# Kernel optimization log

Measured on AMD Instinct MI355X. Metric: run time of the kernel, lower is better.

## Reference

```python
import jax, jax.numpy as jnp
import numpy as np

B, S_RAW, S_SUM, D_IN, H, NH = 32, 1024, 128, 300, 256, 4
DH = (2 * H) // NH  # per-head dim = 128


def _lstm_dir(x, Wih, Whh, b, reverse):
    """Single-direction LSTM (PyTorch gate order i,f,g,o). x: [B,S,D] -> [B,S,H]."""
    xg = jnp.einsum('bsd,gd->bsg', x, Wih) + b          # precompute input gates [B,S,4H]
    xg = jnp.swapaxes(xg, 0, 1)                          # [S,B,4H]
    Hh = Whh.shape[1]
    bsz = x.shape[0]

    def step(carry, g):
        h, c = carry
        gates = g + h @ Whh.T
        i, f, gg, o = jnp.split(gates, 4, axis=-1)
        c = jax.nn.sigmoid(f) * c + jax.nn.sigmoid(i) * jnp.tanh(gg)
        h = jax.nn.sigmoid(o) * jnp.tanh(c)
        return (h, c), h

    init = (jnp.zeros((bsz, Hh), x.dtype), jnp.zeros((bsz, Hh), x.dtype))
    _, hs = jax.lax.scan(step, init, xg, reverse=reverse)  # hs aligned with input time order
    return jnp.swapaxes(hs, 0, 1)


def _bilstm(x, pf, pb):
    return jnp.concatenate([_lstm_dir(x, *pf, False), _lstm_dir(x, *pb, True)], axis=-1)


def setup_inputs() -> dict:
    key = jax.random.key(0)
    ks = jax.random.split(key, 24)
    s_lstm = 1.0 / np.sqrt(H)
    s_proj = 1.0 / np.sqrt(2 * H)
    d = {}
    d['in_raw'] = jax.random.normal(ks[0], (B, S_RAW, D_IN), jnp.float32)
    d['in_sum'] = jax.random.normal(ks[1], (B, S_SUM, D_IN), jnp.float32)
    d['len_raw'] = jax.random.randint(ks[2], (B,), 0, S_RAW)
    d['len_sum'] = jax.random.randint(ks[3], (B,), 0, S_SUM)
    i = 4
    for name in ['raw_f', 'raw_b', 'sum_f', 'sum_b']:
        d[name + '_Wih'] = jax.random.uniform(ks[i], (4 * H, D_IN), jnp.float32, -s_lstm, s_lstm); i += 1
        d[name + '_Whh'] = jax.random.uniform(ks[i], (4 * H, H), jnp.float32, -s_lstm, s_lstm); i += 1
        d[name + '_b'] = jax.random.uniform(ks[i], (4 * H,), jnp.float32, -s_lstm, s_lstm); i += 1
    d['Wq'] = jax.random.uniform(ks[i], (NH, 2 * H, DH), jnp.float32, -s_proj, s_proj); i += 1
    d['Wk'] = jax.random.uniform(ks[i], (NH, 2 * H, DH), jnp.float32, -s_proj, s_proj); i += 1
    d['Wv'] = jax.random.uniform(ks[i], (NH, 2 * H, DH), jnp.float32, -s_proj, s_proj)
    return d


def reference(in_raw, in_sum, len_raw, len_sum,
              raw_f_Wih, raw_f_Whh, raw_f_b, raw_b_Wih, raw_b_Whh, raw_b_b,
              sum_f_Wih, sum_f_Whh, sum_f_b, sum_b_Wih, sum_b_Whh, sum_b_b,
              Wq, Wk, Wv):
    # BiLSTM encoders (dropout is identity in eval mode)
    out_raw = _bilstm(in_raw, (raw_f_Wih, raw_f_Whh, raw_f_b), (raw_b_Wih, raw_b_Whh, raw_b_b))  # [B,Sr,2H]
    out_sum = _bilstm(in_sum, (sum_f_Wih, sum_f_Whh, sum_f_b), (sum_b_Wih, sum_b_Whh, sum_b_b))  # [B,Ss,2H]

    # mean_pooling over the first len_sum[i] timesteps (lengths clamped to >=1)
    lens = jnp.maximum(len_sum, 1)
    mask = (jnp.arange(S_SUM)[None, :] < lens[:, None]).astype(out_sum.dtype)  # [B,Ss]
    sum_vec = jnp.einsum('bsd,bs->bd', out_sum, mask) / lens.astype(out_sum.dtype)[:, None]  # [B,2H]

    # per-head cross-attention against the single pooled summary vector (rank-1 attention)
    q = jnp.einsum('bsd,hde->hbse', out_raw, Wq)   # [NH,B,Sr,DH]
    k = jnp.einsum('bd,hde->hbe', sum_vec, Wk)     # [NH,B,DH]
    v = jnp.einsum('bd,hde->hbe', sum_vec, Wv)     # [NH,B,DH]
    scores = jnp.einsum('hbse,hbe->hbs', q, k)     # [NH,B,Sr] (use_divide_dk=False)
    attn = jax.nn.softmax(scores, axis=-1)
    rst = attn[..., None] * v[:, :, None, :] + q   # outer product + residual, [NH,B,Sr,DH]

    # concat heads along last dim -> [B,Sr,2H]
    rst = jnp.transpose(rst, (1, 2, 0, 3)).reshape(B, S_RAW, NH * DH)
    return rst
```

## Files before the change

kernel.cpp:

```cpp
#include <hip/hip_runtime.h>

typedef _Float16 f16;
typedef _Float16 half2t __attribute__((ext_vector_type(2)));
typedef _Float16 half8 __attribute__((ext_vector_type(8)));
typedef float f32x4 __attribute__((ext_vector_type(4)));

#define KP 320
#define DIN 300
#define SRAW 1024
#define SSUM 128

static constexpr size_t OFF_XG_RAW  = 0;
static constexpr size_t OFF_XG_SUM  = OFF_XG_RAW + (size_t)2*32*1024*1024*2;
static constexpr size_t OFF_OUT_RAW = OFF_XG_SUM + (size_t)2*32*128*1024*2;
static constexpr size_t OFF_OUT_SUM = OFF_OUT_RAW + (size_t)32*1024*512*2;
static constexpr size_t OFF_A_RAW   = OFF_OUT_SUM + (size_t)32*128*512*2;
static constexpr size_t OFF_A_SUM   = OFF_A_RAW + (size_t)32768*KP*2;
static constexpr size_t OFF_BIH_RAW = OFF_A_SUM + (size_t)4096*KP*2;
static constexpr size_t OFF_BIH_SUM = OFF_BIH_RAW + (size_t)2048*KP*2;
static constexpr size_t OFF_WHH     = OFF_BIH_SUM + (size_t)2048*KP*2;
static constexpr size_t OFF_WQ      = OFF_WHH + (size_t)4*32*1024*8*2;
static constexpr size_t OFF_KB      = OFF_WQ + (size_t)512*512*2;
static constexpr size_t OFF_VB      = OFF_KB + (size_t)4*32*128*4;
static constexpr size_t OFF_ATTN    = OFF_VB + (size_t)4*32*128*4;
static constexpr size_t WS_NEED     = OFF_ATTN + (size_t)4*32*1024*4;

__global__ void pack_kernel(
    const float* __restrict__ in_raw, const float* __restrict__ in_sum,
    const float* __restrict__ wih_rf, const float* __restrict__ wih_rb,
    const float* __restrict__ wih_sf, const float* __restrict__ wih_sb,
    const float* __restrict__ whh_rf, const float* __restrict__ whh_rb,
    const float* __restrict__ whh_sf, const float* __restrict__ whh_sb,
    const float* __restrict__ wq,
    f16* __restrict__ a_raw, f16* __restrict__ a_sum,
    f16* __restrict__ bih_raw, f16* __restrict__ bih_sum,
    f16* __restrict__ whh16, f16* __restrict__ wq16)
{
  constexpr size_t N1 = (size_t)32768*KP;
  constexpr size_t N2 = (size_t)4096*KP;
  constexpr size_t N3 = (size_t)2048*KP;
  constexpr size_t N5 = (size_t)4*32*1024*8;
  constexpr size_t N6 = (size_t)512*512;
  const size_t TOT = N1+N2+N3+N3+N5+N6;
  const size_t stride = (size_t)gridDim.x*blockDim.x;
  for (size_t i = (size_t)blockIdx.x*blockDim.x + threadIdx.x; i < TOT; i += stride) {
    size_t j = i;
    if (j < N1) {
      size_t m = j/KP, k = j - m*KP;
      a_raw[j] = (f16)(k < DIN ? in_raw[m*DIN + k] : 0.f);
      continue;
    }
    j -= N1;
    if (j < N2) {
      size_t m = j/KP, k = j - m*KP;
      a_sum[j] = (f16)(k < DIN ? in_sum[m*DIN + k] : 0.f);
      continue;
    }
    j -= N2;
    if (j < N3) {
      size_t n = j/KP, k = j - n*KP;
      float v = 0.f;
      if (k < DIN) v = (n < 1024) ? wih_rf[n*DIN + k] : wih_rb[(n-1024)*DIN + k];
      bih_raw[j] = (f16)v;
      continue;
    }
    j -= N3;
    if (j < N3) {
      size_t n = j/KP, k = j - n*KP;
      float v = 0.f;
      if (k < DIN) v = (n < 1024) ? wih_sf[n*DIN + k] : wih_sb[(n-1024)*DIN + k];
      bih_sum[j] = (f16)v;
      continue;
    }
    j -= N3;
    if (j < N5) {
      int ed = (int)(j >> 18);
      int c  = (int)((j >> 13) & 31);
      int t  = (int)((j >> 3) & 1023);
      int ii = (int)(j & 7);
      int jrow = c >> 2, q = c & 3;
      int rg = t >> 3, ks = t & 7;
      int row = rg*8 + jrow;
      int col = ks*32 + q*8 + ii;
      const float* src = (ed==0)?whh_rf:(ed==1)?whh_rb:(ed==2)?whh_sf:whh_sb;
      whh16[j] = (f16)src[(size_t)row*256 + col];
      continue;
    }
    j -= N5;
    {
      int n = (int)(j >> 9), k = (int)(j & 511);
      int h = n >> 7, dh = n & 127;
      wq16[j] = (f16)wq[((size_t)h*512 + k)*128 + dh];
    }
  }
}

template<int EPI>
__global__ __launch_bounds__(256) void gemm_kernel(
    const f16* __restrict__ A, const f16* __restrict__ Bm,
    float* __restrict__ Cf, f16* __restrict__ Cx,
    const float* __restrict__ bias0, const float* __restrict__ bias1,
    int K, int ldcN, size_t dirStride)
{
  __shared__ __align__(16) f16 As[128*40];
  __shared__ __align__(16) f16 Bs[128*40];
  const int tid = threadIdx.x;
  const int m0 = blockIdx.x*128, n0 = blockIdx.y*128;
  const int w = tid >> 6, lane = tid & 63;
  const int wm = w >> 1, wn = w & 1;
  const int lr = lane & 15, lk = lane >> 4;
  f32x4 acc[4][4] = {};
  const int nsteps = K >> 5;
  for (int kt = 0; kt < nsteps; ++kt) {
    __syncthreads();
    #pragma unroll
    for (int it = 0; it < 2; ++it) {
      int c = tid + it*256;
      int r = c >> 2, kc = c & 3;
      *(uint4*)&As[r*40 + kc*8] = *(const uint4*)&A[(size_t)(m0+r)*K + kt*32 + kc*8];
      *(uint4*)&Bs[r*40 + kc*8] = *(const uint4*)&Bm[(size_t)(n0+r)*K + kt*32 + kc*8];
    }
    __syncthreads();
    half8 af[4], bf[4];
    #pragma unroll
    for (int mt = 0; mt < 4; ++mt) af[mt] = *(const half8*)&As[(wm*64 + mt*16 + lr)*40 + lk*8];
    #pragma unroll
    for (int nt = 0; nt < 4; ++nt) bf[nt] = *(const half8*)&Bs[(wn*64 + nt*16 + lr)*40 + lk*8];
    #pragma unroll
    for (int mt = 0; mt < 4; ++mt)
      #pragma unroll
      for (int nt = 0; nt < 4; ++nt)
        acc[mt][nt] = __builtin_amdgcn_mfma_f32_16x16x32_f16(af[mt], bf[nt], acc[mt][nt], 0, 0, 0);
  }
  const int rb = lk*4;
  #pragma unroll
  for (int mt = 0; mt < 4; ++mt) {
    #pragma unroll
    for (int nt = 0; nt < 4; ++nt) {
      int n = n0 + wn*64 + nt*16 + lr;
      int mloc = m0 + wm*64 + mt*16 + rb;
      if (EPI == 0) {
        #pragma unroll
        for (int r = 0; r < 4; ++r)
          Cf[(size_t)(mloc+r)*ldcN + n] = acc[mt][nt][r];
      } else {
        int dir = n >> 10, cc = n & 1023;
        float bs = (dir ? bias1 : bias0)[cc];
        f16* dst = Cx + (size_t)dir*dirStride;
        #pragma unroll
        for (int r = 0; r < 4; ++r)
          dst[(size_t)(mloc+r)*1024 + cc] = (f16)(acc[mt][nt][r] + bs);
      }
    }
  }
}


__device__ __forceinline__ float dot8(float acc, uint4 wv, uint4 hv) {
#if __has_builtin(__builtin_amdgcn_fdot2)
  union { uint4 u; half2t h[4]; } W, Hh;
  W.u = wv; Hh.u = hv;
  #pragma unroll
  for (int i = 0; i < 4; ++i) acc = __builtin_amdgcn_fdot2(W.h[i], Hh.h[i], acc, false);
#else
  union { uint4 u; f16 h[8]; } W, Hh;
  W.u = wv; Hh.u = hv;
  #pragma unroll
  for (int i = 0; i < 8; ++i) acc += (float)W.h[i]*(float)Hh.h[i];
#endif
  return acc;
}

__device__ __forceinline__ float sigmoid_f(float x) {
  float e = __expf(-x);
  return __builtin_amdgcn_rcpf(1.f + e);
}
__device__ __forceinline__ float tanh_f(float x) {
  float e = __expf(2.f * x);
  return 1.f - 2.f * __builtin_amdgcn_rcpf(e + 1.f);
}

__device__ __forceinline__ void pin4(uint4& v) {
  asm volatile("" : "+v"(v.x), "+v"(v.y), "+v"(v.z), "+v"(v.w));
}

template<int CTRL>
__device__ __forceinline__ float dpp_add(float v) {
  int m = __builtin_amdgcn_update_dpp(0, __builtin_bit_cast(int, v), CTRL, 0xf, 0xf, true);
  return v + __builtin_bit_cast(float, m);
}
__device__ __forceinline__ float reduce8(float v) {
  v = dpp_add<0xB1>(v);
  v = dpp_add<0x4E>(v);
  v = dpp_add<0x141>(v);
  return v;
}

__global__ void __launch_bounds__(1024)
lstm_kernel(
    const f16* __restrict__ whh16,
    const f16* __restrict__ xg_raw, const f16* __restrict__ xg_sum,
    f16* __restrict__ out_raw, f16* __restrict__ out_sum)
{
  const int wg = blockIdx.x;
  const int e = wg >> 6, r2 = wg & 63, d = r2 >> 5, b = r2 & 31;
  const int S = e ? SSUM : SRAW;
  const int t = threadIdx.x;
  const int ks = t & 7;
  const uint4* wb = (const uint4*)(whh16 + (size_t)(e*2+d)*(32*1024*8));
  const f16* xg = (e ? xg_sum : xg_raw) + ((size_t)(d*32 + b))*(size_t)S*1024;
  f16* outp = (e ? out_sum : out_raw) + (size_t)b*S*512 + d*256;

  __shared__ __align__(16) uint4 wl[2*4*1024];
  __shared__ float pre[1024];
  __shared__ __align__(16) f16 hrep[4*264];

  #pragma unroll
  for (int c = 0; c < 8; ++c) wl[c*1024 + t] = wb[(12 + c)*1024 + t];
  uint4 wr[12];
  #pragma unroll
  for (int c = 0; c < 12; ++c) wr[c] = wb[c*1024 + t];
  #pragma unroll
  for (int c = 0; c < 12; ++c) pin4(wr[c]);

  if (t < 256) {
    #pragma unroll
    for (int cpy = 0; cpy < 4; ++cpy) hrep[cpy*264 + t] = (f16)0.f;
  }
  float cst = 0.f;
  const int hbyte = (ks >> 1)*528 + ks*64;
  const bool isG = ((t >> 8) == 2);
  __syncthreads();

  for (int st = 0; st < S; ++st) {
    const int s = d ? (S - 1 - st) : st;

    float xv = (float)xg[(size_t)s*1024 + t];

    uint4 g5[4];
    #pragma unroll
    for (int q = 0; q < 4; ++q) g5[q] = wb[(20 + q)*1024 + t];

    uint4 hv[4];
    #pragma unroll
    for (int q = 0; q < 4; ++q)
      hv[q] = *(const uint4*)((const char*)hrep + hbyte + q*16);

    float pa = 0.f;

    #pragma unroll
    for (int j = 0; j < 3; ++j) {
      float rs = 0.f;
      #pragma unroll
      for (int q = 0; q < 4; ++q) rs = dot8(rs, wr[j*4 + q], hv[q]);
      rs = reduce8(rs);
      pa = (ks == j) ? rs : pa;
    }
    uint4 g6[4];
    #pragma unroll
    for (int q = 0; q < 4; ++q) g6[q] = wb[(24 + q)*1024 + t];
    #pragma unroll
    for (int jj = 0; jj < 2; ++jj) {
      float rs = 0.f;
      #pragma unroll
      for (int q = 0; q < 4; ++q) rs = dot8(rs, wl[(jj*4 + q)*1024 + t], hv[q]);
      rs = reduce8(rs);
      pa = (ks == 3 + jj) ? rs : pa;
    }
    uint4 g7[4];
    #pragma unroll
    for (int q = 0; q < 4; ++q) g7[q] = wb[(28 + q)*1024 + t];
    {
      float rs = 0.f;
      #pragma unroll
      for (int q = 0; q < 4; ++q) rs = dot8(rs, g5[q], hv[q]);
      rs = reduce8(rs);
      pa = (ks == 5) ? rs : pa;
    }
    {
      float rs = 0.f;
      #pragma unroll
      for (int q = 0; q < 4; ++q) rs = dot8(rs, g6[q], hv[q]);
      rs = reduce8(rs);
      pa = (ks == 6) ? rs : pa;
    }
    {
      float rs = 0.f;
      #pragma unroll
      for (int q = 0; q < 4; ++q) rs = dot8(rs, g7[q], hv[q]);
      rs = reduce8(rs);
      pa = (ks == 7) ? rs : pa;
    }

    float v = pa + xv;
    pre[t] = isG ? tanh_f(v) : sigmoid_f(v);
    __syncthreads();

    if (t < 256) {
      float ig = pre[t], fg = pre[256 + t], gg = pre[512 + t], og = pre[768 + t];
      cst = fg*cst + ig*gg;
      float hval = og*tanh_f(cst);
      f16 hf = (f16)hval;
      #pragma unroll
      for (int cpy = 0; cpy < 4; ++cpy) hrep[cpy*264 + t] = hf;
      outp[(size_t)s*512 + t] = hf;
    }
    __syncthreads();
  }
}

__global__ __launch_bounds__(256) void pool_kv_kernel(
    const f16* __restrict__ out_sum, const int* __restrict__ len_sum,
    const float* __restrict__ Wk, const float* __restrict__ Wv,
    float* __restrict__ kb, float* __restrict__ vb)
{
  const int b = blockIdx.x, t = threadIdx.x;
  __shared__ float sv[512];
  int len = len_sum[b]; if (len < 1) len = 1;
  float a0 = 0.f, a1 = 0.f;
  for (int s = 0; s < len; ++s) {
    const f16* row = out_sum + ((size_t)b*SSUM + s)*512;
    a0 += (float)row[t];
    a1 += (float)row[t+256];
  }
  float inv = 1.f/(float)len;
  sv[t] = a0*inv; sv[t+256] = a1*inv;
  __syncthreads();
  #pragma unroll
  for (int half = 0; half < 2; ++half) {
    int o = t + half*256;
    int h = o >> 7, dh = o & 127;
    const float* wkp = Wk + (size_t)h*512*128 + dh;
    const float* wvp = Wv + (size_t)h*512*128 + dh;
    float ak = 0.f, av = 0.f;
    for (int e2 = 0; e2 < 512; ++e2) {
      float sve = sv[e2];
      ak += sve*wkp[(size_t)e2*128];
      av += sve*wvp[(size_t)e2*128];
    }
    kb[((size_t)h*32 + b)*128 + dh] = ak;
    vb[((size_t)h*32 + b)*128 + dh] = av;
  }
}

__global__ __launch_bounds__(256) void attn_kernel(
    const float* __restrict__ q, const float* __restrict__ kb, float* __restrict__ attn)
{
  const int hb = blockIdx.x;
  const int h = hb >> 5, b = hb & 31;
  const int t = threadIdx.x;
  __shared__ __align__(16) float kk[128];
  __shared__ float red[4];
  if (t < 128) kk[t] = kb[(size_t)hb*128 + t];
  __syncthreads();
  float vals[4];
  #pragma unroll
  for (int i = 0; i < 4; ++i) {
    int s = t + i*256;
    const float4* qp = (const float4*)(q + ((size_t)b*1024 + s)*512 + h*128);
    const float4* kp = (const float4*)kk;
    float a = 0.f;
    #pragma unroll
    for (int e2 = 0; e2 < 32; ++e2) {
      float4 qq = qp[e2], kx = kp[e2];
      a += qq.x*kx.x + qq.y*kx.y + qq.z*kx.z + qq.w*kx.w;
    }
    vals[i] = a;
  }
  float m = fmaxf(fmaxf(vals[0], vals[1]), fmaxf(vals[2], vals[3]));
  for (int o = 1; o < 64; o <<= 1) m = fmaxf(m, __shfl_xor(m, o));
  if ((t & 63) == 0) red[t >> 6] = m;
  __syncthreads();
  m = fmaxf(fmaxf(red[0], red[1]), fmaxf(red[2], red[3]));
  __syncthreads();
  float ex[4], lsum = 0.f;
  #pragma unroll
  for (int i = 0; i < 4; ++i) { ex[i] = __expf(vals[i] - m); lsum += ex[i]; }
  for (int o = 1; o < 64; o <<= 1) lsum += __shfl_xor(lsum, o);
  if ((t & 63) == 0) red[t >> 6] = lsum;
  __syncthreads();
  float inv = 1.f/(red[0] + red[1] + red[2] + red[3]);
  #pragma unroll
  for (int i = 0; i < 4; ++i) attn[(size_t)hb*1024 + t + i*256] = ex[i]*inv;
}

__global__ __launch_bounds__(256) void final_kernel(
    float* __restrict__ out, const float* __restrict__ attn, const float* __restrict__ vb)
{
  const size_t TOT4 = (size_t)32*1024*512/4;
  const size_t stride = (size_t)gridDim.x*blockDim.x;
  for (size_t i = (size_t)blockIdx.x*blockDim.x + threadIdx.x; i < TOT4; i += stride) {
    int c4 = (int)(i & 127);
    int h = c4 >> 5;
    size_t srow = i >> 7;
    int b = (int)(srow >> 10), s = (int)(srow & 1023);
    float a = attn[((size_t)h*32 + b)*1024 + s];
    float4 vv = ((const float4*)vb)[((size_t)h*32 + b)*32 + (c4 & 31)];
    float4 qq = ((float4*)out)[i];
    qq.x += a*vv.x; qq.y += a*vv.y; qq.z += a*vv.z; qq.w += a*vv.w;
    ((float4*)out)[i] = qq;
  }
}

extern "C" void kernel_launch(void* const* d_in, const int* in_sizes, int n_in,
                              void* d_out, int out_size, void* d_ws, size_t ws_size,
                              hipStream_t stream)
{
  const float* in_raw = (const float*)d_in[0];
  const float* in_sum = (const float*)d_in[1];
  const int*  len_sum = (const int*)d_in[3];
  const float* rf_wih = (const float*)d_in[4];
  const float* rf_whh = (const float*)d_in[5];
  const float* rf_b   = (const float*)d_in[6];
  const float* rb_wih = (const float*)d_in[7];
  const float* rb_whh = (const float*)d_in[8];
  const float* rb_b   = (const float*)d_in[9];
  const float* sf_wih = (const float*)d_in[10];
  const float* sf_whh = (const float*)d_in[11];
  const float* sf_b   = (const float*)d_in[12];
  const float* sb_wih = (const float*)d_in[13];
  const float* sb_whh = (const float*)d_in[14];
  const float* sb_b   = (const float*)d_in[15];
  const float* wq     = (const float*)d_in[16];
  const float* wk     = (const float*)d_in[17];
  const float* wv     = (const float*)d_in[18];

  if (ws_size < WS_NEED) return;

  char* ws = (char*)d_ws;
  f16* xg_raw_p  = (f16*)(ws + OFF_XG_RAW);
  f16* xg_sum_p  = (f16*)(ws + OFF_XG_SUM);
  f16* out_raw_p = (f16*)(ws + OFF_OUT_RAW);
  f16* out_sum_p = (f16*)(ws + OFF_OUT_SUM);
  f16* a_raw_p   = (f16*)(ws + OFF_A_RAW);
  f16* a_sum_p   = (f16*)(ws + OFF_A_SUM);
  f16* bih_raw_p = (f16*)(ws + OFF_BIH_RAW);
  f16* bih_sum_p = (f16*)(ws + OFF_BIH_SUM);
  f16* whh16_p   = (f16*)(ws + OFF_WHH);
  f16* wq16_p    = (f16*)(ws + OFF_WQ);
  float* kb_p    = (float*)(ws + OFF_KB);
  float* vb_p    = (float*)(ws + OFF_VB);
  float* attn_p  = (float*)(ws + OFF_ATTN);
  float* qout    = (float*)d_out;

  pack_kernel<<<4096, 256, 0, stream>>>(
      in_raw, in_sum, rf_wih, rb_wih, sf_wih, sb_wih,
      rf_whh, rb_whh, sf_whh, sb_whh, wq,
      a_raw_p, a_sum_p, bih_raw_p, bih_sum_p, whh16_p, wq16_p);

  gemm_kernel<1><<<dim3(256, 16), 256, 0, stream>>>(
      a_raw_p, bih_raw_p, nullptr, xg_raw_p, rf_b, rb_b, KP, 0, (size_t)32*1024*1024);
  gemm_kernel<1><<<dim3(32, 16), 256, 0, stream>>>(
      a_sum_p, bih_sum_p, nullptr, xg_sum_p, sf_b, sb_b, KP, 0, (size_t)32*128*1024);

  lstm_kernel<<<128, 1024, 0, stream>>>(whh16_p, xg_raw_p, xg_sum_p, out_raw_p, out_sum_p);

  gemm_kernel<0><<<dim3(256, 4), 256, 0, stream>>>(
      out_raw_p, wq16_p, qout, nullptr, nullptr, nullptr, 512, 512, 0);

  pool_kv_kernel<<<32, 256, 0, stream>>>(out_sum_p, len_sum, wk, wv, kb_p, vb_p);
  attn_kernel<<<128, 256, 0, stream>>>(qout, kb_p, attn_p);
  final_kernel<<<4096, 256, 0, stream>>>(qout, attn_p, vb_p);
}
```

Measured before the change: 2.061 ms.

## Keep more recurrent weights in registers, drop per-step global weight reloads

The LSTM recurrence kernel now holds 24 of 32 weight chunks per thread in registers instead of 12, using the waves_per_eu attribute to permit the larger register budget. The remaining 8 chunks stay in LDS, so the per-step global reloads of 12 weight chunks (g5/g6/g7) are gone. The four padded copies of h in LDS are reduced to a single 256-entry buffer. Risks are register spilling and LDS bank conflicts on the shared h reads.

Result: no change. 2.084 ms (+1.1%).

```diff
diff --git a/kernel.cpp b/kernel.cpp
--- a/kernel.cpp
+++ b/kernel.cpp
@@ -196,7 +196,7 @@
   return v;
 }
 
-__global__ void __launch_bounds__(1024)
+__global__ void __launch_bounds__(1024) __attribute__((amdgpu_waves_per_eu(4, 4)))
 lstm_kernel(
     const f16* __restrict__ whh16,
     const f16* __restrict__ xg_raw, const f16* __restrict__ xg_sum,
@@ -213,22 +213,19 @@
 
   __shared__ __align__(16) uint4 wl[2*4*1024];
   __shared__ float pre[1024];
-  __shared__ __align__(16) f16 hrep[4*264];
-
-  #pragma unroll
-  for (int c = 0; c < 8; ++c) wl[c*1024 + t] = wb[(12 + c)*1024 + t];
-  uint4 wr[12];
-  #pragma unroll
-  for (int c = 0; c < 12; ++c) wr[c] = wb[c*1024 + t];
-  #pragma unroll
-  for (int c = 0; c < 12; ++c) pin4(wr[c]);
-
-  if (t < 256) {
-    #pragma unroll
-    for (int cpy = 0; cpy < 4; ++cpy) hrep[cpy*264 + t] = (f16)0.f;
-  }
+  __shared__ __align__(16) f16 hl[256];
+
+  #pragma unroll
+  for (int c = 0; c < 8; ++c) wl[c*1024 + t] = wb[(24 + c)*1024 + t];
+  uint4 wr[24];
+  #pragma unroll
+  for (int c = 0; c < 24; ++c) wr[c] = wb[c*1024 + t];
+  #pragma unroll
+  for (int c = 0; c < 24; ++c) pin4(wr[c]);
+
+  if (t < 256) hl[t] = (f16)0.f;
   float cst = 0.f;
-  const int hbyte = (ks >> 1)*528 + ks*64;
+  const int hbyte = ks*64;
   const bool isG = ((t >> 8) == 2);
   __syncthreads();
 
@@ -237,59 +234,28 @@
 
     float xv = (float)xg[(size_t)s*1024 + t];
 
-    uint4 g5[4];
-    #pragma unroll
-    for (int q = 0; q < 4; ++q) g5[q] = wb[(20 + q)*1024 + t];
-
     uint4 hv[4];
     #pragma unroll
     for (int q = 0; q < 4; ++q)
-      hv[q] = *(const uint4*)((const char*)hrep + hbyte + q*16);
+      hv[q] = *(const uint4*)((const char*)hl + hbyte + q*16);
 
     float pa = 0.f;
 
     #pragma unroll
-    for (int j = 0; j < 3; ++j) {
+    for (int j = 0; j < 6; ++j) {
       float rs = 0.f;
       #pragma unroll
       for (int q = 0; q < 4; ++q) rs = dot8(rs, wr[j*4 + q], hv[q]);
       rs = reduce8(rs);
       pa = (ks == j) ? rs : pa;
     }
-    uint4 g6[4];
-    #pragma unroll
-    for (int q = 0; q < 4; ++q) g6[q] = wb[(24 + q)*1024 + t];
     #pragma unroll
     for (int jj = 0; jj < 2; ++jj) {
       float rs = 0.f;
       #pragma unroll
       for (int q = 0; q < 4; ++q) rs = dot8(rs, wl[(jj*4 + q)*1024 + t], hv[q]);
       rs = reduce8(rs);
-      pa = (ks == 3 + jj) ? rs : pa;
-    }
-    uint4 g7[4];
-    #pragma unroll
-    for (int q = 0; q < 4; ++q) g7[q] = wb[(28 + q)*1024 + t];
-    {
-      float rs = 0.f;
-      #pragma unroll
-      for (int q = 0; q < 4; ++q) rs = dot8(rs, g5[q], hv[q]);
-      rs = reduce8(rs);
-      pa = (ks == 5) ? rs : pa;
-    }
-    {
-      float rs = 0.f;
-      #pragma unroll
-      for (int q = 0; q < 4; ++q) rs = dot8(rs, g6[q], hv[q]);
-      rs = reduce8(rs);
-      pa = (ks == 6) ? rs : pa;
-    }
-    {
-      float rs = 0.f;
-      #pragma unroll
-      for (int q = 0; q < 4; ++q) rs = dot8(rs, g7[q], hv[q]);
-      rs = reduce8(rs);
-      pa = (ks == 7) ? rs : pa;
+      pa = (ks == 6 + jj) ? rs : pa;
     }
 
     float v = pa + xv;
@@ -301,8 +267,7 @@
       cst = fg*cst + ig*gg;
       float hval = og*tanh_f(cst);
       f16 hf = (f16)hval;
-      #pragma unroll
-      for (int cpy = 0; cpy < 4; ++cpy) hrep[cpy*264 + t] = hf;
+      hl[t] = hf;
       outp[(size_t)s*512 + t] = hf;
     }
     __syncthreads();
```
